# Performance work log

Hardware: AMD Instinct MI355X
Metric: run time of the kernel (lower is better)

The kernel has to match this reference:

```python
import jax, jax.numpy as jnp
import numpy as np

N_NODES = 50000
N_EDGES = 800000
N_GRAPHS = 256
NODE_IN = 92
EDGE_IN = 41
H = 128
N_CONV = 3
N_HID = 2
N_PROP = 3

sp = jax.nn.softplus


def _lin_init(key, fan_in, fan_out):
    kw, kb = jax.random.split(key)
    bound = 1.0 / np.sqrt(fan_in)
    W = jax.random.uniform(kw, (fan_in, fan_out), jnp.float32, -bound, bound)
    b = jax.random.uniform(kb, (fan_out,), jnp.float32, -bound, bound)
    return W, b


def setup_inputs() -> dict:
    key = jax.random.key(0)
    ks = jax.random.split(key, 32)
    x = jax.random.normal(ks[0], (N_NODES, NODE_IN), jnp.float32)
    edge_attr = jax.random.uniform(ks[1], (N_EDGES, EDGE_IN), jnp.float32)
    edge_index = jax.random.randint(ks[2], (2, N_EDGES), 0, N_NODES, jnp.int32)
    batch = jnp.sort(jax.random.randint(ks[3], (N_NODES,), 0, N_GRAPHS, jnp.int32))

    node_W, node_b = _lin_init(ks[4], NODE_IN, H)
    edge_W, edge_b = _lin_init(ks[5], EDGE_IN, H)

    # Stacked conv-layer params over N_CONV layers
    e1 = [_lin_init(jax.random.fold_in(ks[6], i), 3 * H, 2 * H) for i in range(N_CONV)]
    e2 = [_lin_init(jax.random.fold_in(ks[7], i), 2 * H, H) for i in range(N_CONV)]
    nn_ = [_lin_init(jax.random.fold_in(ks[8], i), 2 * H, H) for i in range(N_CONV)]
    conv_e1_W = jnp.stack([w for w, _ in e1]); conv_e1_b = jnp.stack([b for _, b in e1])
    conv_e2_W = jnp.stack([w for w, _ in e2]); conv_e2_b = jnp.stack([b for _, b in e2])
    conv_n_W = jnp.stack([w for w, _ in nn_]); conv_n_b = jnp.stack([b for _, b in nn_])

    shared_W1, shared_b1 = _lin_init(ks[9], H, H)
    shared_W2, shared_b2 = _lin_init(ks[10], H, H)

    # Stacked task-head params: [n_prop, n_hidden, H, H] + output [n_prop, H, 1]
    hW, hb, hoW, hob = [], [], [], []
    for p in range(N_PROP):
        ws, bs = [], []
        for l in range(N_HID):
            w, b = _lin_init(jax.random.fold_in(ks[11], p * 10 + l), H, H)
            ws.append(w); bs.append(b)
        hW.append(jnp.stack(ws)); hb.append(jnp.stack(bs))
        w, b = _lin_init(jax.random.fold_in(ks[12], p), H, 1)
        hoW.append(w); hob.append(b)
    head_W = jnp.stack(hW); head_b = jnp.stack(hb)
    head_out_W = jnp.stack(hoW); head_out_b = jnp.stack(hob)

    return dict(x=x, edge_attr=edge_attr, node_W=node_W, node_b=node_b,
                edge_W=edge_W, edge_b=edge_b,
                conv_e1_W=conv_e1_W, conv_e1_b=conv_e1_b,
                conv_e2_W=conv_e2_W, conv_e2_b=conv_e2_b,
                conv_n_W=conv_n_W, conv_n_b=conv_n_b,
                shared_W1=shared_W1, shared_b1=shared_b1,
                shared_W2=shared_W2, shared_b2=shared_b2,
                head_W=head_W, head_b=head_b,
                head_out_W=head_out_W, head_out_b=head_out_b,
                edge_index=edge_index, batch=batch)


def reference(x, edge_attr, node_W, node_b, edge_W, edge_b,
              conv_e1_W, conv_e1_b, conv_e2_W, conv_e2_b, conv_n_W, conv_n_b,
              shared_W1, shared_b1, shared_W2, shared_b2,
              head_W, head_b, head_out_W, head_out_b,
              edge_index, batch):
    row, col = edge_index[0], edge_index[1]
    h = x @ node_W + node_b                      # [N, H]
    ea = edge_attr @ edge_W + edge_b             # [E, H]

    for i in range(N_CONV):
        # gather node pairs -> edge MLP
        edge_input = jnp.concatenate([h[row], h[col], ea], axis=-1)   # [E, 3H]
        ee = sp(edge_input @ conv_e1_W[i] + conv_e1_b[i])             # [E, 2H]
        ee = sp(ee @ conv_e2_W[i] + conv_e2_b[i])                     # [E, H]
        # scatter-add aggregate into destination nodes (col)
        aggr = jax.ops.segment_sum(ee, col, num_segments=N_NODES)     # [N, H]
        node_input = jnp.concatenate([h, aggr], axis=-1)              # [N, 2H]
        h = sp(node_input @ conv_n_W[i] + conv_n_b[i]) + h            # residual

    # global mean pool per graph
    sums = jax.ops.segment_sum(h, batch, num_segments=N_GRAPHS)       # [B, H]
    counts = jax.ops.segment_sum(jnp.ones((h.shape[0], 1), h.dtype), batch,
                                 num_segments=N_GRAPHS)               # [B, 1]
    g = sums / jnp.maximum(counts, 1.0)

    g = sp(g @ shared_W1 + shared_b1)
    g = sp(g @ shared_W2 + shared_b2)                                 # [B, H]

    # task heads, vectorized over properties
    t = jnp.broadcast_to(g, (N_PROP,) + g.shape)                      # [P, B, H]
    for l in range(N_HID):
        t = sp(jnp.einsum('pbd,pdh->pbh', t, head_W[:, l]) + head_b[:, l][:, None, :])
    out = jnp.einsum('pbd,pdo->pbo', t, head_out_W) + head_out_b[:, None, :]
    return out[..., 0]                                                # [P, B]
```

## Files before the change

kernel.cpp:

```cpp
#include <hip/hip_runtime.h>

typedef _Float16 half_t;
typedef __attribute__((ext_vector_type(8))) _Float16 h8_t;
typedef __attribute__((ext_vector_type(4))) _Float16 h4_t;
typedef __attribute__((ext_vector_type(4))) float f4_t;

#define NN      50000
#define NE      800000
#define NG      256
#define NODE_IN 92
#define EDGE_IN 41

__device__ __forceinline__ float softplus_f(float x) {
  return fmaxf(x, 0.0f) + __logf(1.0f + __expf(-fabsf(x)));
}
__device__ __forceinline__ unsigned pk2(float a, float b) {
  return __builtin_bit_cast(unsigned, __builtin_amdgcn_cvt_pkrtz(a, b));
}

__global__ __launch_bounds__(256) void prep_weights_kernel(
    const float* __restrict__ e1W, const float* __restrict__ e2W,
    const float* __restrict__ nW,
    half_t* __restrict__ W1T, half_t* __restrict__ W2T, half_t* __restrict__ WnT)
{
  int idx = blockIdx.x * 256 + threadIdx.x;
  if (idx < 294912) {
    int i = idx / 98304, rem = idx % 98304;
    int n = rem / 384, k = rem % 384;
    W1T[idx] = (half_t)e1W[i * 98304 + k * 256 + n];
  } else if (idx < 393216) {
    int o = idx - 294912;
    int i = o / 32768, rem = o % 32768;
    int n = rem / 256, k = rem % 256;
    W2T[o] = (half_t)e2W[i * 32768 + k * 128 + n];
  } else {
    int o = idx - 393216;
    int i = o / 32768, rem = o % 32768;
    int n = rem / 256, k = rem % 256;
    WnT[o] = (half_t)nW[i * 32768 + k * 128 + n];
  }
}

__global__ __launch_bounds__(256) void prep_comp_kernel(
    const float* __restrict__ e1W, const float* __restrict__ e1b,
    const float* __restrict__ eW, const float* __restrict__ eb,
    half_t* __restrict__ WcT, float* __restrict__ b1c)
{
  int idx = blockIdx.x * 256 + threadIdx.x;
  if (idx < 49152) {
    int L = idx / 16384, rem = idx % 16384;
    int n = rem / 64, k = rem % 64;
    float s = 0.f;
    if (k < EDGE_IN) {
      const float* w1 = e1W + (size_t)L * 98304 + 256 * 256 + n;
      const float* we = eW + k * 128;
      for (int j = 0; j < 128; ++j) s += we[j] * w1[(size_t)j * 256];
    }
    WcT[idx] = (half_t)s;
  } else if (idx < 49920) {
    int o = idx - 49152;
    int L = o / 256, n = o % 256;
    float s = e1b[L * 256 + n];
    const float* w1 = e1W + (size_t)L * 98304 + 256 * 256 + n;
    for (int j = 0; j < 128; ++j) s += eb[j] * w1[(size_t)j * 256];
    b1c[o] = s;
  }
}

__global__ __launch_bounds__(256) void node_embed_kernel(
    const float* __restrict__ x, const float* __restrict__ W,
    const float* __restrict__ bias, float* __restrict__ hf,
    half_t* __restrict__ h16)
{
  __shared__ float xs[16 * NODE_IN];
  int n0 = blockIdx.x * 16;
  for (int i = threadIdx.x; i < 16 * NODE_IN; i += 256)
    xs[i] = x[(size_t)n0 * NODE_IN + i];
  __syncthreads();
  int ch = threadIdx.x & 127, g = threadIdx.x >> 7;
  float acc[8] = {0.f,0.f,0.f,0.f,0.f,0.f,0.f,0.f};
  for (int k = 0; k < NODE_IN; ++k) {
    float w = W[k * 128 + ch];
    #pragma unroll
    for (int u = 0; u < 8; ++u) acc[u] += xs[(g + 2*u) * NODE_IN + k] * w;
  }
  float bv = bias[ch];
  #pragma unroll
  for (int u = 0; u < 8; ++u) {
    int n = n0 + g + 2*u;
    float v = acc[u] + bv;
    hf[(size_t)n*128 + ch] = v;
    h16[(size_t)n*128 + ch] = (half_t)v;
  }
}

__global__ __launch_bounds__(256) void ea_convert_kernel(
    const float* __restrict__ ea, const int* __restrict__ ipos,
    half_t* __restrict__ eaF)
{
  __shared__ float es[64 * EDGE_IN];
  __shared__ int sip[64];
  int e0 = blockIdx.x * 64;
  for (int i = threadIdx.x; i < 64 * EDGE_IN; i += 256)
    es[i] = ea[(size_t)e0 * EDGE_IN + i];
  if (threadIdx.x < 64) sip[threadIdx.x] = ipos[e0 + threadIdx.x];
  __syncthreads();
  #pragma unroll
  for (int it = 0; it < 2; ++it) {
    int idx = threadIdx.x + it * 256;
    int e = idx >> 3, c = idx & 7;
    int c0 = c * 8;
    float f[8];
    #pragma unroll
    for (int j = 0; j < 8; ++j) {
      int col = c0 + j;
      f[j] = (col < EDGE_IN) ? es[e * EDGE_IN + col] : 0.f;
    }
    uint4 pk;
    pk.x = pk2(f[0], f[1]); pk.y = pk2(f[2], f[3]);
    pk.z = pk2(f[4], f[5]); pk.w = pk2(f[6], f[7]);
    *reinterpret_cast<uint4*>(eaF + (size_t)sip[e] * 64 + c0) = pk;
  }
}

__global__ __launch_bounds__(256) void csr_count_kernel(
    const int* __restrict__ col, int* __restrict__ cnt)
{
  int e = blockIdx.x * 256 + threadIdx.x;
  atomicAdd(&cnt[col[e]], 1);
}

__global__ __launch_bounds__(256) void scan_block_kernel(
    const int* __restrict__ cnt, int* __restrict__ cur, int* __restrict__ bsum)
{
  __shared__ int buf[256];
  int t = threadIdx.x;
  int i = blockIdx.x * 256 + t;
  int v = (i < NN) ? cnt[i] : 0;
  buf[t] = v;
  __syncthreads();
  for (int off = 1; off < 256; off <<= 1) {
    int y = (t >= off) ? buf[t - off] : 0;
    __syncthreads();
    buf[t] += y;
    __syncthreads();
  }
  if (i < NN) cur[i] = buf[t] - v;
  if (t == 255) bsum[blockIdx.x] = buf[255];
}

__global__ __launch_bounds__(256) void scan_top_kernel(
    const int* __restrict__ bsum, int* __restrict__ bbase, int nblk)
{
  __shared__ int buf[256];
  int t = threadIdx.x;
  int v = (t < nblk) ? bsum[t] : 0;
  buf[t] = v;
  __syncthreads();
  for (int off = 1; off < 256; off <<= 1) {
    int y = (t >= off) ? buf[t - off] : 0;
    __syncthreads();
    buf[t] += y;
    __syncthreads();
  }
  if (t < nblk) bbase[t] = buf[t] - v;
}

__global__ __launch_bounds__(256) void scan_add_kernel(
    int* __restrict__ cur, const int* __restrict__ bbase)
{
  int i = blockIdx.x * 256 + threadIdx.x;
  if (i < NN) cur[i] += bbase[blockIdx.x];
}

__global__ __launch_bounds__(256) void csr_fill_kernel(
    const int* __restrict__ row, const int* __restrict__ col,
    int* __restrict__ cur,
    int* __restrict__ rowv, int* __restrict__ colv, int* __restrict__ ipos)
{
  int e = blockIdx.x * 256 + threadIdx.x;
  int c = col[e];
  int pos = atomicAdd(&cur[c], 1);
  rowv[pos] = row[e];
  colv[pos] = c;
  ipos[e] = pos;
}

__global__ __launch_bounds__(256) void uv_kernel(
    const half_t* __restrict__ h16, const half_t* __restrict__ W1T,
    const float* __restrict__ b1c,
    half_t* __restrict__ u16, half_t* __restrict__ v16)
{
  __shared__ char smem[64 * 256];
  const int tid = threadIdx.x;
  const int n0 = blockIdx.x * 64;

  #pragma unroll
  for (int it = 0; it < 4; ++it) {
    int idx = tid + it * 256;
    int r = idx >> 4, c = idx & 15;
    int node = n0 + r;
    uint4 w = make_uint4(0u, 0u, 0u, 0u);
    if (node < NN) w = *reinterpret_cast<const uint4*>(h16 + (size_t)node * 128 + c * 8);
    unsigned o = (unsigned)(r * 256 + c * 16) ^ (unsigned)((r & 7) << 4);
    *reinterpret_cast<uint4*>(smem + o) = w;
  }
  __syncthreads();

  const int lane = tid & 63, wave = tid >> 6;
  const int lr = lane & 15, lg = lane >> 4;

  #pragma unroll
  for (int pass = 0; pass < 2; ++pass) {
    const half_t* Ww = W1T + (size_t)(wave * 64) * 384 + pass * 128;
    f4_t acc[4][4] = {};
    for (int ks = 0; ks < 4; ++ks) {
      h8_t a[4], b[4];
      #pragma unroll
      for (int m = 0; m < 4; ++m)
        a[m] = *reinterpret_cast<const h8_t*>(Ww + (size_t)(m * 16 + lr) * 384 + ks * 32 + lg * 8);
      #pragma unroll
      for (int n = 0; n < 4; ++n) {
        int r = n * 16 + lr;
        unsigned o = (unsigned)(r * 256 + ks * 64 + lg * 16) ^ (unsigned)((r & 7) << 4);
        b[n] = *reinterpret_cast<const h8_t*>(smem + o);
      }
      #pragma unroll
      for (int m = 0; m < 4; ++m)
        #pragma unroll
        for (int n = 0; n < 4; ++n)
          acc[m][n] = __builtin_amdgcn_mfma_f32_16x16x32_f16(a[m], b[n], acc[m][n], 0, 0, 0);
    }
    half_t* dst = pass ? v16 : u16;
    #pragma unroll
    for (int m = 0; m < 4; ++m) {
      int chb = wave * 64 + m * 16 + lg * 4;
      float bb0 = 0.f, bb1 = 0.f, bb2 = 0.f, bb3 = 0.f;
      if (pass == 0) { bb0 = b1c[chb]; bb1 = b1c[chb+1]; bb2 = b1c[chb+2]; bb3 = b1c[chb+3]; }
      #pragma unroll
      for (int n = 0; n < 4; ++n) {
        int node = n0 + n * 16 + lr;
        if (node < NN) {
          uint2 pk;
          pk.x = pk2(acc[m][n][0] + bb0, acc[m][n][1] + bb1);
          pk.y = pk2(acc[m][n][2] + bb2, acc[m][n][3] + bb3);
          *reinterpret_cast<uint2*>(dst + (size_t)node * 256 + chb) = pk;
        }
      }
    }
  }
}

__global__ __launch_bounds__(512, 8) void conv_edge_kernel(
    const half_t* __restrict__ u16, const half_t* __restrict__ v16,
    const half_t* __restrict__ eaF,
    const int* __restrict__ rowv, const int* __restrict__ colv,
    const half_t* __restrict__ WcT,
    const half_t* __restrict__ W2T, const float* __restrict__ b2,
    float* __restrict__ aggrF)
{
  __shared__ char smem[64 * 512 + 64 * 128];
  const int tid = threadIdx.x;

  const int nwg = gridDim.x;
  const int q = nwg >> 3, r = nwg & 7;
  const int xcd = blockIdx.x & 7, slot = blockIdx.x >> 3;
  const int swz = (xcd < r ? xcd * (q + 1) : r * (q + 1) + (xcd - r) * q) + slot;
  const int e0 = swz * 64;

  #pragma unroll
  for (int it = 0; it < 4; ++it) {
    int idx = tid + it * 512;
    int e = idx >> 5, c = idx & 31;
    int nr = rowv[e0 + e], nc = colv[e0 + e];
    h8_t su = *reinterpret_cast<const h8_t*>(u16 + (size_t)nr * 256 + c * 8);
    h8_t sv = *reinterpret_cast<const h8_t*>(v16 + (size_t)nc * 256 + c * 8);
    h8_t s = su + sv;
    unsigned o = (unsigned)(e * 512 + c * 16) ^ (unsigned)((e & 7) << 4);
    *reinterpret_cast<h8_t*>(smem + o) = s;
  }
  {
    int e = tid >> 3, c = tid & 7;
    uint4 w = *reinterpret_cast<const uint4*>(eaF + (size_t)(e0 + e) * 64 + c * 8);
    unsigned o = (unsigned)(32768 + e * 128 + c * 16) ^ (unsigned)((e & 7) << 4);
    *reinterpret_cast<uint4*>(smem + o) = w;
  }
  __syncthreads();

  const int lane = tid & 63, wave = tid >> 6;
  const int lr = lane & 15, lg = lane >> 4;

  const half_t* W1w = WcT + (size_t)(wave * 32) * 64;
  #pragma unroll
  for (int pass = 0; pass < 2; ++pass) {
    f4_t acc[2][2] = {};
    #pragma unroll
    for (int ks = 0; ks < 2; ++ks) {
      h8_t a[2], b[2];
      #pragma unroll
      for (int m = 0; m < 2; ++m)
        a[m] = *reinterpret_cast<const h8_t*>(W1w + (size_t)(m * 16 + lr) * 64 + ks * 32 + lg * 8);
      #pragma unroll
      for (int n = 0; n < 2; ++n) {
        int e = pass * 32 + n * 16 + lr;
        unsigned o = (unsigned)(32768 + e * 128 + ks * 64 + lg * 16) ^ (unsigned)((e & 7) << 4);
        b[n] = *reinterpret_cast<const h8_t*>(smem + o);
      }
      #pragma unroll
      for (int m = 0; m < 2; ++m)
        #pragma unroll
        for (int n = 0; n < 2; ++n)
          acc[m][n] = __builtin_amdgcn_mfma_f32_16x16x32_f16(a[m], b[n], acc[m][n], 0, 0, 0);
    }
    #pragma unroll
    for (int m = 0; m < 2; ++m) {
      int chb = wave * 32 + m * 16 + lg * 4;
      #pragma unroll
      for (int n = 0; n < 2; ++n) {
        int e = pass * 32 + n * 16 + lr;
        unsigned o = (unsigned)(e * 512 + chb * 2) ^ (unsigned)((e & 7) << 4);
        h4_t s = *reinterpret_cast<const h4_t*>(smem + o);
        float v0 = softplus_f(acc[m][n][0] + (float)s[0]);
        float v1 = softplus_f(acc[m][n][1] + (float)s[1]);
        float v2 = softplus_f(acc[m][n][2] + (float)s[2]);
        float v3 = softplus_f(acc[m][n][3] + (float)s[3]);
        uint2 pk;
        pk.x = pk2(v0, v1);
        pk.y = pk2(v2, v3);
        *reinterpret_cast<uint2*>(smem + o) = pk;
      }
    }
  }
  __syncthreads();

  const half_t* W2w = W2T + (size_t)(wave * 16) * 256;
  f4_t acc2[4] = {};
  for (int ks = 0; ks < 8; ++ks) {
    h8_t a2 = *reinterpret_cast<const h8_t*>(W2w + (size_t)lr * 256 + ks * 32 + lg * 8);
    h8_t b2v[4];
    #pragma unroll
    for (int n = 0; n < 4; ++n) {
      int e = n * 16 + lr;
      unsigned o = (unsigned)(e * 512 + ks * 64 + lg * 16) ^ (unsigned)((e & 7) << 4);
      b2v[n] = *reinterpret_cast<const h8_t*>(smem + o);
    }
    #pragma unroll
    for (int n = 0; n < 4; ++n)
      acc2[n] = __builtin_amdgcn_mfma_f32_16x16x32_f16(a2, b2v[n], acc2[n], 0, 0, 0);
  }
  __syncthreads();

  {
    if (tid < 64)
      *reinterpret_cast<int*>(smem + 32768 + tid * 4) = colv[e0 + tid];
    int chb = wave * 16 + lg * 4;
    float bb0 = b2[chb + 0], bb1 = b2[chb + 1], bb2 = b2[chb + 2], bb3 = b2[chb + 3];
    #pragma unroll
    for (int n = 0; n < 4; ++n) {
      int e = n * 16 + lr;
      float4 v;
      v.x = softplus_f(acc2[n][0] + bb0);
      v.y = softplus_f(acc2[n][1] + bb1);
      v.z = softplus_f(acc2[n][2] + bb2);
      v.w = softplus_f(acc2[n][3] + bb3);
      unsigned o = (unsigned)(e * 512 + chb * 4) ^ (unsigned)((e & 7) << 4);
      *reinterpret_cast<float4*>(smem + o) = v;
    }
  }
  __syncthreads();

  {
    const int* scol = reinterpret_cast<const int*>(smem + 32768);
    int ch = tid & 127, g2 = tid >> 7;
    int ebase = g2 * 16;
    float a = 0.f;
    int curc = scol[ebase];
    #pragma unroll
    for (int k = 0; k < 16; ++k) {
      int e = ebase + k;
      int c = scol[e];
      if (c != curc) {
        atomicAdd(&aggrF[(size_t)curc * 128 + ch], a);
        a = 0.f; curc = c;
      }
      unsigned o = (unsigned)(e * 512 + ch * 4) ^ (unsigned)((e & 7) << 4);
      a += *reinterpret_cast<const float*>(smem + o);
    }
    atomicAdd(&aggrF[(size_t)curc * 128 + ch], a);
  }
}

__global__ __launch_bounds__(512, 4) void conv_node_kernel(
    half_t* __restrict__ h16, const float* __restrict__ aggrF,
    const half_t* __restrict__ WnT, const float* __restrict__ bn,
    float* __restrict__ hf)
{
  __shared__ char smem[64 * 256 * 2];
  const int tid = threadIdx.x;
  const int n0 = blockIdx.x * 64;

  #pragma unroll
  for (int it = 0; it < 4; ++it) {
    int idx = tid + it * 512;
    int r = idx >> 5, c = idx & 31;
    int node = n0 + r;
    uint4 v = make_uint4(0u, 0u, 0u, 0u);
    if (node < NN) {
      if (c < 16) {
        v = *reinterpret_cast<const uint4*>(h16 + (size_t)node * 128 + c * 8);
      } else {
        const float* src = aggrF + (size_t)node * 128 + (c - 16) * 8;
        float4 f0 = *reinterpret_cast<const float4*>(src);
        float4 f1 = *reinterpret_cast<const float4*>(src + 4);
        v.x = pk2(f0.x, f0.y); v.y = pk2(f0.z, f0.w);
        v.z = pk2(f1.x, f1.y); v.w = pk2(f1.z, f1.w);
      }
    }
    unsigned o = (unsigned)(r * 512 + c * 16) ^ (unsigned)((r & 7) << 4);
    *reinterpret_cast<uint4*>(smem + o) = v;
  }
  __syncthreads();

  const int lane = tid & 63, wave = tid >> 6;
  const int lr = lane & 15, lg = lane >> 4;
  const int c0 = wave * 16;
  f4_t acc[4] = {};
  for (int ks = 0; ks < 8; ++ks) {
    h8_t a[4], b;
    #pragma unroll
    for (int m = 0; m < 4; ++m) {
      int row = m * 16 + lr;
      unsigned o = (unsigned)(row * 512 + ks * 64 + lg * 16) ^ (unsigned)((row & 7) << 4);
      a[m] = *reinterpret_cast<const h8_t*>(smem + o);
    }
    b = *reinterpret_cast<const h8_t*>(WnT + (size_t)(c0 + lr) * 256 + ks * 32 + lg * 8);
    #pragma unroll
    for (int m = 0; m < 4; ++m)
      acc[m] = __builtin_amdgcn_mfma_f32_16x16x32_f16(a[m], b, acc[m], 0, 0, 0);
  }
  #pragma unroll
  for (int m = 0; m < 4; ++m)
    #pragma unroll
    for (int r = 0; r < 4; ++r) {
      int row = m * 16 + lg * 4 + r;
      int col = c0 + lr;
      int node = n0 + row;
      if (node < NN) {
        float v = softplus_f(acc[m][r] + bn[col]) + hf[(size_t)node * 128 + col];
        hf[(size_t)node * 128 + col] = v;
        h16[(size_t)node * 128 + col] = (half_t)v;
      }
    }
}

__global__ __launch_bounds__(128) void pool_kernel(
    const float* __restrict__ hf, const int* __restrict__ batch,
    float* __restrict__ gsum, int* __restrict__ gcnt)
{
  int t = threadIdx.x;
  int n0 = blockIdx.x * 16;
  float acc = 0.f;
  int curb = batch[n0];
  for (int i = 0; i < 16; ++i) {
    int n = n0 + i;
    int b = batch[n];
    if (b != curb) { atomicAdd(&gsum[curb * 128 + t], acc); acc = 0.f; curb = b; }
    acc += hf[(size_t)n * 128 + t];
  }
  atomicAdd(&gsum[curb * 128 + t], acc);
  if (t == 0) {
    int c = 0, cb = batch[n0];
    for (int i = 0; i < 16; ++i) {
      int b = batch[n0 + i];
      if (b != cb) { atomicAdd(&gcnt[cb], c); c = 0; cb = b; }
      ++c;
    }
    atomicAdd(&gcnt[cb], c);
  }
}

__global__ __launch_bounds__(128) void heads_kernel(
    const float* __restrict__ gsum, const int* __restrict__ gcnt,
    const float* __restrict__ sW1, const float* __restrict__ sb1,
    const float* __restrict__ sW2, const float* __restrict__ sb2,
    const float* __restrict__ hW, const float* __restrict__ hb,
    const float* __restrict__ hoW, const float* __restrict__ hob,
    float* __restrict__ out)
{
  int b = blockIdx.x, t = threadIdx.x;
  __shared__ float va[128], vb[128], vc[128], red[128];
  float inv = 1.0f / fmaxf((float)gcnt[b], 1.0f);
  va[t] = gsum[b * 128 + t] * inv;
  __syncthreads();
  { float a = 0.f;
    for (int k = 0; k < 128; ++k) a += va[k] * sW1[k * 128 + t];
    float r = softplus_f(a + sb1[t]);
    __syncthreads(); vb[t] = r; __syncthreads(); }
  { float a = 0.f;
    for (int k = 0; k < 128; ++k) a += vb[k] * sW2[k * 128 + t];
    float r = softplus_f(a + sb2[t]);
    __syncthreads(); va[t] = r; __syncthreads(); }
  for (int p = 0; p < 3; ++p) {
    { float a = 0.f;
      for (int k = 0; k < 128; ++k) a += va[k] * hW[((p * 2 + 0) * 128 + k) * 128 + t];
      float r = softplus_f(a + hb[(p * 2 + 0) * 128 + t]);
      __syncthreads(); vb[t] = r; __syncthreads(); }
    { float a = 0.f;
      for (int k = 0; k < 128; ++k) a += vb[k] * hW[((p * 2 + 1) * 128 + k) * 128 + t];
      float r = softplus_f(a + hb[(p * 2 + 1) * 128 + t]);
      __syncthreads(); vc[t] = r; __syncthreads(); }
    red[t] = vc[t] * hoW[p * 128 + t];
    __syncthreads();
    for (int s = 64; s > 0; s >>= 1) {
      if (t < s) red[t] += red[t + s];
      __syncthreads();
    }
    if (t == 0) out[p * NG + b] = red[0] + hob[p];
    __syncthreads();
  }
}

extern "C" void kernel_launch(void* const* d_in, const int* in_sizes, int n_in,
                              void* d_out, int out_size, void* d_ws, size_t ws_size,
                              hipStream_t stream)
{
  const float* x     = (const float*)d_in[0];
  const float* eattr = (const float*)d_in[1];
  const float* nodeW = (const float*)d_in[2];
  const float* nodeb = (const float*)d_in[3];
  const float* edgeW = (const float*)d_in[4];
  const float* edgeb = (const float*)d_in[5];
  const float* e1W   = (const float*)d_in[6];
  const float* e1b   = (const float*)d_in[7];
  const float* e2W   = (const float*)d_in[8];
  const float* e2b   = (const float*)d_in[9];
  const float* nW    = (const float*)d_in[10];
  const float* nb    = (const float*)d_in[11];
  const float* sW1   = (const float*)d_in[12];
  const float* sb1   = (const float*)d_in[13];
  const float* sW2   = (const float*)d_in[14];
  const float* sb2   = (const float*)d_in[15];
  const float* hW    = (const float*)d_in[16];
  const float* hb    = (const float*)d_in[17];
  const float* hoW   = (const float*)d_in[18];
  const float* hob   = (const float*)d_in[19];
  const int*   eidx  = (const int*)d_in[20];
  const int*   batch = (const int*)d_in[21];
  float* out = (float*)d_out;

  char* base = (char*)d_ws;
  size_t woff = 0;
  auto alloc = [&](size_t bytes) -> char* {
    char* r = base + woff;
    woff = (woff + bytes + 255) & ~(size_t)255;
    return r;
  };
  float*  hf     = (float*) alloc((size_t)NN * 128 * 4);
  half_t* h16    = (half_t*)alloc((size_t)NN * 128 * 2);
  half_t* eaF    = (half_t*)alloc((size_t)NE * 64 * 2);
  float*  aggrF  = (float*) alloc((size_t)NN * 128 * 4);
  half_t* u16    = (half_t*)alloc((size_t)NN * 256 * 2);
  half_t* v16    = (half_t*)alloc((size_t)NN * 256 * 2);
  half_t* W1T    = (half_t*)alloc((size_t)3 * 256 * 384 * 2);
  half_t* W2T    = (half_t*)alloc((size_t)3 * 128 * 256 * 2);
  half_t* WnT    = (half_t*)alloc((size_t)3 * 128 * 256 * 2);
  half_t* WcT    = (half_t*)alloc((size_t)3 * 256 * 64 * 2);
  float*  b1c    = (float*) alloc((size_t)3 * 256 * 4);
  int* cnt    = (int*)alloc((size_t)NN * 4);
  int* cur    = (int*)alloc((size_t)NN * 4);
  int* bsum   = (int*)alloc(256 * 4);
  int* bbase  = (int*)alloc(256 * 4);
  int* rowv   = (int*)alloc((size_t)NE * 4);
  int* colv   = (int*)alloc((size_t)NE * 4);
  int* ipos   = (int*)alloc((size_t)NE * 4);
  float* gsum = (float*)alloc((size_t)NG * 128 * 4);
  int*   gcnt = (int*)alloc((size_t)NG * 4);
  if (woff > ws_size) return;

  const int NSCAN = (NN + 255) / 256;

  hipMemsetAsync(cnt, 0, (size_t)NN * 4, stream);
  hipMemsetAsync(gsum, 0, (size_t)NG * 128 * 4, stream);
  hipMemsetAsync(gcnt, 0, (size_t)NG * 4, stream);

  csr_count_kernel<<<NE / 256, 256, 0, stream>>>(eidx + NE, cnt);
  scan_block_kernel<<<NSCAN, 256, 0, stream>>>(cnt, cur, bsum);
  scan_top_kernel<<<1, 256, 0, stream>>>(bsum, bbase, NSCAN);
  scan_add_kernel<<<NSCAN, 256, 0, stream>>>(cur, bbase);
  csr_fill_kernel<<<NE / 256, 256, 0, stream>>>(eidx, eidx + NE, cur, rowv, colv, ipos);

  prep_weights_kernel<<<1920, 256, 0, stream>>>(e1W, e2W, nW, W1T, W2T, WnT);
  prep_comp_kernel<<<195, 256, 0, stream>>>(e1W, e1b, edgeW, edgeb, WcT, b1c);
  node_embed_kernel<<<NN / 16, 256, 0, stream>>>(x, nodeW, nodeb, hf, h16);
  ea_convert_kernel<<<NE / 64, 256, 0, stream>>>(eattr, ipos, eaF);

  for (int L = 0; L < 3; ++L) {
    hipMemsetAsync(aggrF, 0, (size_t)NN * 128 * 4, stream);
    uv_kernel<<<(NN + 63) / 64, 256, 0, stream>>>(
        h16, W1T + (size_t)L * 98304, b1c + (size_t)L * 256, u16, v16);
    conv_edge_kernel<<<NE / 64, 512, 0, stream>>>(
        u16, v16, eaF, rowv, colv,
        WcT + (size_t)L * 16384,
        W2T + (size_t)L * 32768, e2b + (size_t)L * 128, aggrF);
    conv_node_kernel<<<(NN + 63) / 64, 512, 0, stream>>>(
        h16, aggrF, WnT + (size_t)L * 32768, nb + (size_t)L * 128, hf);
  }
  pool_kernel<<<NN / 16, 128, 0, stream>>>(hf, batch, gsum, gcnt);
  heads_kernel<<<NG, 128, 0, stream>>>(gsum, gcnt, sW1, sb1, sW2, sb2,
                                       hW, hb, hoW, hob, out);
}
```

Baseline: 1.156 ms.

## Fuse next-layer UV projection and mean-pool into conv node kernel

The conv node kernel now stages the updated fp16 node features in shared memory and runs the next layer's U/V projection right away, so the separate uv_kernel launches for layers two and three are removed. It also avoids re-reading h16 from global memory for that projection. In the last layer the kernel atomically adds its outputs into per-graph sums instead of writing hf, which replaces the separate pool kernel; graph counts move to a small atomic kernel. The cost is a heavier epilogue with more registers, extra syncs, and many fine-grained float atomics on gsum.

```diff
diff --git a/kernel.cpp b/kernel.cpp
--- a/kernel.cpp
+++ b/kernel.cpp
@@ -186,6 +186,13 @@
   ipos[e] = pos;
 }
 
+__global__ __launch_bounds__(256) void gcnt_kernel(
+    const int* __restrict__ batch, int* __restrict__ gcnt)
+{
+  int i = blockIdx.x * 256 + threadIdx.x;
+  if (i < NN) atomicAdd(&gcnt[batch[i]], 1);
+}
+
 __global__ __launch_bounds__(256) void uv_kernel(
     const half_t* __restrict__ h16, const half_t* __restrict__ W1T,
     const float* __restrict__ b1c,
@@ -390,14 +397,24 @@
   }
 }
 
+template<int MODE>
 __global__ __launch_bounds__(512, 4) void conv_node_kernel(
     half_t* __restrict__ h16, const float* __restrict__ aggrF,
     const half_t* __restrict__ WnT, const float* __restrict__ bn,
-    float* __restrict__ hf)
+    float* __restrict__ hf,
+    const half_t* __restrict__ W1Tn, const float* __restrict__ b1cn,
+    half_t* __restrict__ u16, half_t* __restrict__ v16,
+    const int* __restrict__ batch, float* __restrict__ gsum)
 {
   __shared__ char smem[64 * 256 * 2];
+  __shared__ int sbatch[64];
   const int tid = threadIdx.x;
   const int n0 = blockIdx.x * 64;
+
+  if (MODE == 1 && tid < 64) {
+    int node = n0 + tid;
+    sbatch[tid] = (node < NN) ? batch[node] : 0;
+  }
 
   #pragma unroll
   for (int it = 0; it < 4; ++it) {
@@ -438,44 +455,79 @@
     for (int m = 0; m < 4; ++m)
       acc[m] = __builtin_amdgcn_mfma_f32_16x16x32_f16(a[m], b, acc[m], 0, 0, 0);
   }
-  #pragma unroll
-  for (int m = 0; m < 4; ++m)
-    #pragma unroll
-    for (int r = 0; r < 4; ++r) {
-      int row = m * 16 + lg * 4 + r;
-      int col = c0 + lr;
-      int node = n0 + row;
-      if (node < NN) {
-        float v = softplus_f(acc[m][r] + bn[col]) + hf[(size_t)node * 128 + col];
-        hf[(size_t)node * 128 + col] = v;
-        h16[(size_t)node * 128 + col] = (half_t)v;
-      }
-    }
-}
-
-__global__ __launch_bounds__(128) void pool_kernel(
-    const float* __restrict__ hf, const int* __restrict__ batch,
-    float* __restrict__ gsum, int* __restrict__ gcnt)
-{
-  int t = threadIdx.x;
-  int n0 = blockIdx.x * 16;
-  float acc = 0.f;
-  int curb = batch[n0];
-  for (int i = 0; i < 16; ++i) {
-    int n = n0 + i;
-    int b = batch[n];
-    if (b != curb) { atomicAdd(&gsum[curb * 128 + t], acc); acc = 0.f; curb = b; }
-    acc += hf[(size_t)n * 128 + t];
-  }
-  atomicAdd(&gsum[curb * 128 + t], acc);
-  if (t == 0) {
-    int c = 0, cb = batch[n0];
-    for (int i = 0; i < 16; ++i) {
-      int b = batch[n0 + i];
-      if (b != cb) { atomicAdd(&gcnt[cb], c); c = 0; cb = b; }
-      ++c;
-    }
-    atomicAdd(&gcnt[cb], c);
+  __syncthreads();
+
+  if (MODE == 1) {
+    #pragma unroll
+    for (int m = 0; m < 4; ++m)
+      #pragma unroll
+      for (int r = 0; r < 4; ++r) {
+        int row = m * 16 + lg * 4 + r;
+        int col = c0 + lr;
+        int node = n0 + row;
+        if (node < NN) {
+          float v = softplus_f(acc[m][r] + bn[col]) + hf[(size_t)node * 128 + col];
+          atomicAdd(&gsum[(size_t)sbatch[row] * 128 + col], v);
+        }
+      }
+  } else {
+    #pragma unroll
+    for (int m = 0; m < 4; ++m)
+      #pragma unroll
+      for (int r = 0; r < 4; ++r) {
+        int row = m * 16 + lg * 4 + r;
+        int col = c0 + lr;
+        int node = n0 + row;
+        half_t hv = (half_t)0.f;
+        if (node < NN) {
+          float v = softplus_f(acc[m][r] + bn[col]) + hf[(size_t)node * 128 + col];
+          hf[(size_t)node * 128 + col] = v;
+          hv = (half_t)v;
+          h16[(size_t)node * 128 + col] = hv;
+        }
+        unsigned o = (unsigned)(row * 256 + col * 2) ^ (unsigned)((row & 7) << 4);
+        *reinterpret_cast<half_t*>(smem + o) = hv;
+      }
+    __syncthreads();
+
+    const int pass = wave >> 2;
+    const int ch0 = (wave & 3) * 64;
+    const half_t* Ww = W1Tn + (size_t)ch0 * 384 + pass * 128;
+    f4_t acc2[4][4] = {};
+    for (int ks = 0; ks < 4; ++ks) {
+      h8_t a[4], b[4];
+      #pragma unroll
+      for (int m = 0; m < 4; ++m)
+        a[m] = *reinterpret_cast<const h8_t*>(Ww + (size_t)(m * 16 + lr) * 384 + ks * 32 + lg * 8);
+      #pragma unroll
+      for (int n = 0; n < 4; ++n) {
+        int r = n * 16 + lr;
+        unsigned o = (unsigned)(r * 256 + ks * 64 + lg * 16) ^ (unsigned)((r & 7) << 4);
+        b[n] = *reinterpret_cast<const h8_t*>(smem + o);
+      }
+      #pragma unroll
+      for (int m = 0; m < 4; ++m)
+        #pragma unroll
+        for (int n = 0; n < 4; ++n)
+          acc2[m][n] = __builtin_amdgcn_mfma_f32_16x16x32_f16(a[m], b[n], acc2[m][n], 0, 0, 0);
+    }
+    half_t* dst = pass ? v16 : u16;
+    #pragma unroll
+    for (int m = 0; m < 4; ++m) {
+      int chb = ch0 + m * 16 + lg * 4;
+      float bb0 = 0.f, bb1 = 0.f, bb2 = 0.f, bb3 = 0.f;
+      if (pass == 0) { bb0 = b1cn[chb]; bb1 = b1cn[chb+1]; bb2 = b1cn[chb+2]; bb3 = b1cn[chb+3]; }
+      #pragma unroll
+      for (int n = 0; n < 4; ++n) {
+        int node = n0 + n * 16 + lr;
+        if (node < NN) {
+          uint2 pk;
+          pk.x = pk2(acc2[m][n][0] + bb0, acc2[m][n][1] + bb1);
+          pk.y = pk2(acc2[m][n][2] + bb2, acc2[m][n][3] + bb3);
+          *reinterpret_cast<uint2*>(dst + (size_t)node * 256 + chb) = pk;
+        }
+      }
+    }
   }
 }
 
@@ -578,6 +630,7 @@
   if (woff > ws_size) return;
 
   const int NSCAN = (NN + 255) / 256;
+  const int NBLK  = (NN + 63) / 64;
 
   hipMemsetAsync(cnt, 0, (size_t)NN * 4, stream);
   hipMemsetAsync(gsum, 0, (size_t)NG * 128 * 4, stream);
@@ -588,24 +641,33 @@
   scan_top_kernel<<<1, 256, 0, stream>>>(bsum, bbase, NSCAN);
   scan_add_kernel<<<NSCAN, 256, 0, stream>>>(cur, bbase);
   csr_fill_kernel<<<NE / 256, 256, 0, stream>>>(eidx, eidx + NE, cur, rowv, colv, ipos);
+  gcnt_kernel<<<NSCAN, 256, 0, stream>>>(batch, gcnt);
 
   prep_weights_kernel<<<1920, 256, 0, stream>>>(e1W, e2W, nW, W1T, W2T, WnT);
   prep_comp_kernel<<<195, 256, 0, stream>>>(e1W, e1b, edgeW, edgeb, WcT, b1c);
   node_embed_kernel<<<NN / 16, 256, 0, stream>>>(x, nodeW, nodeb, hf, h16);
   ea_convert_kernel<<<NE / 64, 256, 0, stream>>>(eattr, ipos, eaF);
 
+  uv_kernel<<<NBLK, 256, 0, stream>>>(h16, W1T, b1c, u16, v16);
+
   for (int L = 0; L < 3; ++L) {
     hipMemsetAsync(aggrF, 0, (size_t)NN * 128 * 4, stream);
-    uv_kernel<<<(NN + 63) / 64, 256, 0, stream>>>(
-        h16, W1T + (size_t)L * 98304, b1c + (size_t)L * 256, u16, v16);
     conv_edge_kernel<<<NE / 64, 512, 0, stream>>>(
         u16, v16, eaF, rowv, colv,
         WcT + (size_t)L * 16384,
         W2T + (size_t)L * 32768, e2b + (size_t)L * 128, aggrF);
-    conv_node_kernel<<<(NN + 63) / 64, 512, 0, stream>>>(
-        h16, aggrF, WnT + (size_t)L * 32768, nb + (size_t)L * 128, hf);
-  }
-  pool_kernel<<<NN / 16, 128, 0, stream>>>(hf, batch, gsum, gcnt);
+    if (L < 2) {
+      conv_node_kernel<0><<<NBLK, 512, 0, stream>>>(
+          h16, aggrF, WnT + (size_t)L * 32768, nb + (size_t)L * 128, hf,
+          W1T + (size_t)(L + 1) * 98304, b1c + (size_t)(L + 1) * 256, u16, v16,
+          nullptr, nullptr);
+    } else {
+      conv_node_kernel<1><<<NBLK, 512, 0, stream>>>(
+          h16, aggrF, WnT + (size_t)L * 32768, nb + (size_t)L * 128, hf,
+          nullptr, nullptr, nullptr, nullptr,
+          batch, gsum);
+    }
+  }
   heads_kernel<<<NG, 128, 0, stream>>>(gsum, gcnt, sW1, sb1, sW2, sb2,
                                        hW, hb, hoW, hob, out);
 }
```

After: 1.288 ms. 11.4% more time.
